# Kernel tuning notes

Hardware: AMD Instinct MI355X
Metric: run time of the kernel (lower is better)

Reference implementation:

```python
import jax, jax.numpy as jnp
import numpy as np
import math

B, T, C, H = 2, 2048, 1024, 16
D = C // H  # head dim = 64


def setup_inputs() -> dict:
    key = jax.random.key(0)
    ks = jax.random.split(key, 9)
    s = 1.0 / math.sqrt(C)
    inp = {
        "x": jax.random.normal(ks[0], (B, T, C), dtype=jnp.float32),
        "Wk": jax.random.normal(ks[1], (C, C), dtype=jnp.float32) * s,
        "bk": jax.random.normal(ks[2], (C,), dtype=jnp.float32) * s,
        "Wq": jax.random.normal(ks[3], (C, C), dtype=jnp.float32) * s,
        "bq": jax.random.normal(ks[4], (C,), dtype=jnp.float32) * s,
        "Wv": jax.random.normal(ks[5], (C, C), dtype=jnp.float32) * s,
        "bv": jax.random.normal(ks[6], (C,), dtype=jnp.float32) * s,
        "Wo": jax.random.normal(ks[7], (C, C), dtype=jnp.float32) * s,
        "bo": jax.random.normal(ks[8], (C,), dtype=jnp.float32) * s,
    }
    return inp


def reference(x, Wk, bk, Wq, bq, Wv, bv, Wo, bo):
    # QKV projections, split heads: [B,T,C] -> [B,H,T,D]
    def proj(W, b):
        return (x @ W.T + b).reshape(B, T, H, D).transpose(0, 2, 1, 3)

    k = proj(Wk, bk)
    q = proj(Wq, bq)
    v = proj(Wv, bv)

    # NOTE: original scales by 1/sqrt(embedding_dim), not head_dim
    scale = 1.0 / math.sqrt(C)
    scores = jnp.einsum("bhtd,bhsd->bhts", q, k) * scale  # [B,H,T,T]
    causal = jnp.tril(jnp.ones((T, T), dtype=bool))
    scores = jnp.where(causal[None, None], scores, -jnp.inf)
    attn = jax.nn.softmax(scores, axis=-1)
    y = jnp.einsum("bhts,bhsd->bhtd", attn, v)  # [B,H,T,D]
    y = y.transpose(0, 2, 1, 3).reshape(B, T, C)
    return y @ Wo.T + bo
```

## Files before the change

kernel.cpp:

```cpp
#include <hip/hip_runtime.h>
#include <hip/hip_bf16.h>
#include <stdint.h>
#include <stddef.h>

#define B_ 2
#define T_ 2048
#define C_ 1024
#define H_ 16
#define D_ 64
#define M_ (B_*T_)

typedef __attribute__((ext_vector_type(8))) short short8;
typedef __attribute__((ext_vector_type(4))) float f32x4;
typedef __attribute__((ext_vector_type(16))) float f32x16;
typedef __attribute__((ext_vector_type(4))) unsigned int u32x4;

__device__ __forceinline__ unsigned short f2bf(float f) {
    unsigned u = __float_as_uint(f);
    unsigned r = 0x7FFFu + ((u >> 16) & 1u);
    return (unsigned short)((u + r) >> 16);
}

__device__ __forceinline__ unsigned cvtpk_bf16(float lo, float hi) {
    unsigned r;
    asm("v_cvt_pk_bf16_f32 %0, %1, %2" : "=v"(r) : "v"(lo), "v"(hi));
    return r;
}

__device__ __forceinline__ float fexp2(float x) {
    float r;
    asm("v_exp_f32 %0, %1" : "=v"(r) : "v"(x));
    return r;
}

__device__ __forceinline__ void plswap(unsigned &a, unsigned &b) {
    asm("v_permlane32_swap_b32 %0, %1" : "+v"(a), "+v"(b));
}

__device__ __forceinline__ float xhalf_max(float v) {
    float a = v, b = v;
    asm("" : "+v"(b));
    asm("v_permlane32_swap_b32 %0, %1" : "+v"(a), "+v"(b));
    return fmaxf(a, b);
}
__device__ __forceinline__ float xhalf_sum(float v) {
    float a = v, b = v;
    asm("" : "+v"(b));
    asm("v_permlane32_swap_b32 %0, %1" : "+v"(a), "+v"(b));
    return a + b;
}

__device__ __forceinline__ void gload16(const void* g, void* l) {
    __builtin_amdgcn_global_load_lds(
        (__attribute__((address_space(1))) void*)g,
        (__attribute__((address_space(3))) void*)l,
        16, 0, 0);
}

__global__ void cvt_all(const float* __restrict__ x,  const float* __restrict__ wk,
                        const float* __restrict__ wq, const float* __restrict__ wv,
                        const float* __restrict__ wo,
                        unsigned short* __restrict__ xb,  unsigned short* __restrict__ wkb,
                        unsigned short* __restrict__ wqb, unsigned short* __restrict__ wvb,
                        unsigned short* __restrict__ wob) {
    int idx = (blockIdx.x * blockDim.x + threadIdx.x) * 4;
    const float* in; unsigned short* out; int off;
    if      (idx < (4<<20)) { in = x;  out = xb;  off = idx; }
    else if (idx < (5<<20)) { in = wk; out = wkb; off = idx - (4<<20); }
    else if (idx < (6<<20)) { in = wq; out = wqb; off = idx - (5<<20); }
    else if (idx < (7<<20)) { in = wv; out = wvb; off = idx - (6<<20); }
    else                    { in = wo; out = wob; off = idx - (7<<20); }
    float4 v = *reinterpret_cast<const float4*>(in + off);
    ushort4 o;
    o.x = f2bf(v.x); o.y = f2bf(v.y); o.z = f2bf(v.z); o.w = f2bf(v.w);
    *reinterpret_cast<ushort4*>(out + off) = o;
}

__global__ __launch_bounds__(256) void gemm_qkv(
    const unsigned short* __restrict__ A,
    const unsigned short* __restrict__ W0,
    const unsigned short* __restrict__ W1,
    const unsigned short* __restrict__ W2,
    const float* __restrict__ b0,
    const float* __restrict__ b1,
    const float* __restrict__ b2,
    unsigned short* __restrict__ o0,
    unsigned short* __restrict__ o1,
    unsigned short* __restrict__ o2)
{
    __shared__ unsigned short As[128*32];
    __shared__ unsigned short Bs[128*32];
    int which = blockIdx.x >> 8;
    int bx = blockIdx.x & 255;
    int bm = bx >> 3, bn = bx & 7;
    const unsigned short* W = (which==0) ? W0 : ((which==1) ? W1 : W2);
    const float* bias = (which==0) ? b0 : ((which==1) ? b1 : b2);

    int tid = threadIdx.x;
    int lane = tid & 63;
    int fr = lane & 15, fq = lane >> 4;
    int wid = tid >> 6;
    int wr = wid >> 1, wc = wid & 1;

    int srow = tid >> 2;
    int scol = (tid & 3) << 3;
    const unsigned short* Ab = A + (size_t)(bm*128 + srow) * C_ + scol;
    const unsigned short* Wb = W + (size_t)(bn*128 + srow) * C_ + scol;

    f32x4 acc[4][4] = {};

    for (int kt = 0; kt < C_/32; ++kt) {
        int ko = kt*32;
        gload16(Ab + ko,            &As[tid*8]);
        gload16(Ab + 64*C_ + ko,    &As[2048 + tid*8]);
        gload16(Wb + ko,            &Bs[tid*8]);
        gload16(Wb + 64*C_ + ko,    &Bs[2048 + tid*8]);
        __syncthreads();
        short8 af[4], bfr[4];
        #pragma unroll
        for (int i = 0; i < 4; ++i) {
            af[i]  = *reinterpret_cast<const short8*>(&As[(wr*64 + i*16 + fr)*32 + fq*8]);
            bfr[i] = *reinterpret_cast<const short8*>(&Bs[(wc*64 + i*16 + fr)*32 + fq*8]);
        }
        #pragma unroll
        for (int i = 0; i < 4; ++i)
            #pragma unroll
            for (int j = 0; j < 4; ++j)
                acc[i][j] = __builtin_amdgcn_mfma_f32_16x16x32_bf16(af[i], bfr[j], acc[i][j], 0, 0, 0);
        __syncthreads();
    }

    float sc = (which == 1) ? 0.045084220f : 1.0f;
    int mbase = bm*128 + wr*64;
    int nbase = bn*128 + wc*64;
    #pragma unroll
    for (int j = 0; j < 4; ++j) {
        int col = nbase + j*16 + fr;
        float bv = bias[col];
        int h = col >> 6, d = col & 63;
        #pragma unroll
        for (int i = 0; i < 4; ++i) {
            int r0 = mbase + i*16 + fq*4;
            #pragma unroll
            for (int r = 0; r < 4; ++r) {
                float v = (acc[i][j][r] + bv) * sc;
                int m = r0 + r;
                int b = m >> 11, t = m & (T_-1);
                unsigned short hv = f2bf(v);
                if (which == 2)
                    o2[((size_t)(b*H_ + h)*D_ + d)*T_ + t] = hv;
                else {
                    unsigned short* o = (which==0) ? o0 : o1;
                    o[((size_t)(b*H_ + h)*T_ + t)*D_ + d] = hv;
                }
            }
        }
    }
}

__global__ __launch_bounds__(256, 6) void gemm_out(
    const unsigned short* __restrict__ A,
    const unsigned short* __restrict__ W,
    const float* __restrict__ bias,
    float* __restrict__ out)
{
    __shared__ unsigned short As[64*32];
    __shared__ unsigned short Bs[128*32];
    int bx = blockIdx.x;
    int bm = bx >> 3, bn = bx & 7;

    int tid = threadIdx.x;
    int lane = tid & 63;
    int fr = lane & 15, fq = lane >> 4;
    int wid = tid >> 6;
    int wr = wid >> 1, wc = wid & 1;

    int arow = tid >> 2;
    int acol = (tid & 3) << 3;
    const unsigned short* Ab = A + (size_t)(bm*64 + arow) * C_ + acol;
    const unsigned short* Wb = W + (size_t)(bn*128 + arow) * C_ + acol;

    f32x4 acc[2][4] = {};

    for (int kt = 0; kt < C_/32; ++kt) {
        int ko = kt*32;
        gload16(Ab + ko,            &As[tid*8]);
        gload16(Wb + ko,            &Bs[tid*8]);
        gload16(Wb + 64*C_ + ko,    &Bs[2048 + tid*8]);
        __syncthreads();
        short8 af[2], bfr[4];
        #pragma unroll
        for (int i = 0; i < 2; ++i)
            af[i]  = *reinterpret_cast<const short8*>(&As[(wr*32 + i*16 + fr)*32 + fq*8]);
        #pragma unroll
        for (int j = 0; j < 4; ++j)
            bfr[j] = *reinterpret_cast<const short8*>(&Bs[(wc*64 + j*16 + fr)*32 + fq*8]);
        #pragma unroll
        for (int i = 0; i < 2; ++i)
            #pragma unroll
            for (int j = 0; j < 4; ++j)
                acc[i][j] = __builtin_amdgcn_mfma_f32_16x16x32_bf16(af[i], bfr[j], acc[i][j], 0, 0, 0);
        __syncthreads();
    }

    int mbase = bm*64 + wr*32;
    int nbase = bn*128 + wc*64;
    #pragma unroll
    for (int j = 0; j < 4; ++j) {
        int col = nbase + j*16 + fr;
        float bv = bias[col];
        #pragma unroll
        for (int i = 0; i < 2; ++i) {
            int r0 = mbase + i*16 + fq*4;
            #pragma unroll
            for (int r = 0; r < 4; ++r)
                out[(size_t)(r0 + r)*C_ + col] = acc[i][j][r] + bv;
        }
    }
}

__device__ __forceinline__ void attn_subtile(
    const short8 (&kf)[4], const short8 (&qf)[4],
    const short8 (&vlo)[2], const short8 (&vhi)[2],
    bool diag, int l31, int hi,
    f32x16& o0, f32x16& o1, float& m_, float& l_)
{
    f32x16 a0 = {};
    __builtin_amdgcn_s_setprio(1);
    a0 = __builtin_amdgcn_mfma_f32_32x32x16_bf16(kf[0], qf[0], a0, 0, 0, 0);
    a0 = __builtin_amdgcn_mfma_f32_32x32x16_bf16(kf[1], qf[1], a0, 0, 0, 0);
    a0 = __builtin_amdgcn_mfma_f32_32x32x16_bf16(kf[2], qf[2], a0, 0, 0, 0);
    a0 = __builtin_amdgcn_mfma_f32_32x32x16_bf16(kf[3], qf[3], a0, 0, 0, 0);
    __builtin_amdgcn_s_setprio(0);

    if (diag) {
        #pragma unroll
        for (int r = 0; r < 16; ++r) {
            int kvl = (r&3) + 8*(r>>2) + 4*hi;
            if (kvl > l31) a0[r] = -1e30f;
        }
    }

    float x0 = fmaxf(a0[0], a0[1]),   x1 = fmaxf(a0[2], a0[3]);
    float x2 = fmaxf(a0[4], a0[5]),   x3 = fmaxf(a0[6], a0[7]);
    float x4 = fmaxf(a0[8], a0[9]),   x5 = fmaxf(a0[10], a0[11]);
    float x6 = fmaxf(a0[12], a0[13]), x7 = fmaxf(a0[14], a0[15]);
    float y0 = fmaxf(x0, x1), y1 = fmaxf(x2, x3), y2 = fmaxf(x4, x5), y3 = fmaxf(x6, x7);
    float pm = fmaxf(fmaxf(y0, y1), fmaxf(y2, y3));
    pm = xhalf_max(pm);

    if (!__all(pm - m_ <= 8.0f)) {
        float mn = fmaxf(m_, pm);
        float alpha = fexp2(m_ - mn);
        l_ *= alpha;
        m_ = mn;
        #pragma unroll
        for (int r = 0; r < 16; ++r) {
            int row = (r&3) + 8*(r>>2) + 4*hi;
            float ar = __shfl(alpha, row);
            o0[r] *= ar;
            o1[r] *= ar;
        }
    }

    #pragma unroll
    for (int r = 0; r < 16; ++r)
        a0[r] = fexp2(a0[r] - m_);
    float s0 = a0[0]+a0[1],  s1 = a0[2]+a0[3],  s2 = a0[4]+a0[5],   s3 = a0[6]+a0[7];
    float s4 = a0[8]+a0[9],  s5 = a0[10]+a0[11], s6 = a0[12]+a0[13], s7 = a0[14]+a0[15];
    float u0 = s0+s1, u1 = s2+s3, u2 = s4+s5, u3 = s6+s7;
    float rs = (u0+u1) + (u2+u3);
    rs = xhalf_sum(rs);
    l_ += rs;

    unsigned pk_[8];
    #pragma unroll
    for (int jj = 0; jj < 8; ++jj)
        pk_[jj] = cvtpk_bf16(a0[2*jj], a0[2*jj+1]);

    #pragma unroll
    for (int kb = 0; kb < 2; ++kb) {
        unsigned fx = pk_[4*kb+0], fz = pk_[4*kb+2];
        unsigned fy = pk_[4*kb+1], fw = pk_[4*kb+3];
        plswap(fx, fz);
        plswap(fy, fw);
        u32x4 wv;
        wv.x = fx; wv.y = fy; wv.z = fz; wv.w = fw;
        short8 pfrag = __builtin_bit_cast(short8, wv);
        __builtin_amdgcn_s_setprio(1);
        o0 = __builtin_amdgcn_mfma_f32_32x32x16_bf16(pfrag, vlo[kb], o0, 0, 0, 0);
        o1 = __builtin_amdgcn_mfma_f32_32x32x16_bf16(pfrag, vhi[kb], o1, 0, 0, 0);
        __builtin_amdgcn_s_setprio(0);
    }
}

__global__ __launch_bounds__(256, 4) void flash_attn(
    const unsigned short* __restrict__ q,
    const unsigned short* __restrict__ k,
    const unsigned short* __restrict__ vt,
    unsigned short* __restrict__ y)
{
    __shared__ __align__(16) char LDSRAW[35840];
    unsigned short (*ST)[4][2048] = reinterpret_cast<unsigned short(*)[4][2048]>(LDSRAW);
    float* oP = reinterpret_cast<float*>(LDSRAW);
    float* mP = oP + 4*32*68;
    float* lP = mP + 128;

    int tid = threadIdx.x, lane = tid & 63, w = tid >> 6;
    int l31 = lane & 31, hi = lane >> 5, rsw = l31 & 7;
    int p = w & 1, s = w >> 1;
    int bid = blockIdx.x;

    int half = bid >> 9;
    int idx  = bid & 511;
    int bh   = (idx & 7)*4 + ((idx >> 3) & 3);
    int jidx = idx >> 5;
    int j    = half ? jidx : (31 - jidx);

    const unsigned short* kp = k  + (size_t)bh*T_*D_;
    const unsigned short* vp = vt + (size_t)bh*D_*T_;
    int b = bh >> 4, h = bh & 15;

    int rowbase = j*64 + p*32;
    const unsigned short* qp = q + ((size_t)bh*T_ + rowbase) * D_;

    short8 qf[4];
    #pragma unroll
    for (int dk = 0; dk < 4; ++dk)
        qf[dk] = *reinterpret_cast<const short8*>(qp + (size_t)l31*D_ + dk*16 + hi*8);

    f32x16 o0 = {}, o1 = {};
    float m_ = -1e30f, l_ = 0.f;

    int lim = 2*j + p;
    int niter = j + 1;
    int gbase = s ? (j + 1) : 0;

    #define STAGE(ii, bufi)                                                           \
    {                                                                                 \
        int c2 = tid;                                                                 \
        int krow = c2 >> 3;                                                           \
        int kslot = (c2 & 7) ^ (krow & 7);                                            \
        int vrow = c2 >> 2;                                                           \
        int vslot = (c2 & 3) ^ (vrow & 3);                                            \
        int tl_ = (ii), th_ = j + 1 + (ii);                                           \
        gload16(kp + ((size_t)(tl_*32 + krow))*D_ + kslot*8, &ST[bufi][0][c2*8]);     \
        gload16(kp + ((size_t)(th_*32 + krow))*D_ + kslot*8, &ST[bufi][1][c2*8]);     \
        gload16(vp + (size_t)vrow*T_ + tl_*32 + vslot*8,     &ST[bufi][2][c2*8]);     \
        gload16(vp + (size_t)vrow*T_ + th_*32 + vslot*8,     &ST[bufi][3][c2*8]);     \
    }

    STAGE(0, 0);
    __syncthreads();

    for (int i = 0; i < niter; ++i) {
        int bufi = i & 1;
        if (i + 1 < niter) STAGE(i + 1, bufi ^ 1);

        int g = gbase + i;
        if (g <= lim) {
            const unsigned short* Kl = &ST[bufi][s][0];
            const unsigned short* Vl = &ST[bufi][2 + s][0];
            short8 kf[4];
            #pragma unroll
            for (int dk = 0; dk < 4; ++dk)
                kf[dk] = *reinterpret_cast<const short8*>(
                    Kl + l31*64 + ((((dk<<1)|hi)) ^ rsw)*8);
            short8 vlo[2], vhi[2];
            #pragma unroll
            for (int kb = 0; kb < 2; ++kb) {
                int sl = ((((kb<<1)|hi)) ^ (l31 & 3)) * 8;
                vlo[kb] = *reinterpret_cast<const short8*>(Vl + l31*32 + sl);
                vhi[kb] = *reinterpret_cast<const short8*>(Vl + (32 + l31)*32 + sl);
            }
            attn_subtile(kf, qf, vlo, vhi, g == lim, l31, hi, o0, o1, m_, l_);
        }
        __syncthreads();
    }
    #undef STAGE

    {
        int set = (s << 1) | p;
        #pragma unroll
        for (int rr = 0; rr < 16; ++rr) {
            int crow = (rr&3) + 8*(rr>>2) + 4*hi;
            oP[(set*32 + crow)*68 + l31]      = o0[rr];
            oP[(set*32 + crow)*68 + 32 + l31] = o1[rr];
        }
        if (!hi) { mP[set*32 + l31] = m_; lP[set*32 + l31] = l_; }
    }
    __syncthreads();
    {
        int qr = tid >> 3;
        int dc = tid & 7;
        #pragma unroll
        for (int ch = 0; ch < 2; ++ch) {
            int sA = ch, sB = 2 + ch;
            float mA = mP[sA*32 + qr], mB = mP[sB*32 + qr];
            float lA = lP[sA*32 + qr], lB = lP[sB*32 + qr];
            float mN = fmaxf(mA, mB);
            float aA = fexp2(mA - mN);
            float aB = fexp2(mB - mN);
            float lN = lA*aA + lB*aB;
            float inv = 1.0f / lN;
            float cA = aA * inv, cB = aB * inv;

            unsigned short yv[8];
            #pragma unroll
            for (int e = 0; e < 8; ++e) {
                float acc = cA * oP[(sA*32 + qr)*68 + dc*8 + e]
                          + cB * oP[(sB*32 + qr)*68 + dc*8 + e];
                yv[e] = f2bf(acc);
            }
            int trow = j*64 + ch*32 + qr;
            size_t base = ((size_t)(b*T_ + trow))*C_ + h*64 + dc*8;
            *reinterpret_cast<short8*>(y + base) = *reinterpret_cast<short8*>(yv);
        }
    }
}

extern "C" void kernel_launch(void* const* d_in, const int* in_sizes, int n_in,
                              void* d_out, int out_size, void* d_ws, size_t ws_size,
                              hipStream_t stream) {
    const float* x  = (const float*)d_in[0];
    const float* Wk = (const float*)d_in[1];
    const float* bk = (const float*)d_in[2];
    const float* Wq = (const float*)d_in[3];
    const float* bq = (const float*)d_in[4];
    const float* Wv = (const float*)d_in[5];
    const float* bv = (const float*)d_in[6];
    const float* Wo = (const float*)d_in[7];
    const float* bo = (const float*)d_in[8];
    float* out = (float*)d_out;

    char* ws = (char*)d_ws;
    unsigned short* xb  = (unsigned short*)(ws);
    unsigned short* wkb = (unsigned short*)(ws + ((size_t)8  << 20));
    unsigned short* wqb = (unsigned short*)(ws + ((size_t)10 << 20));
    unsigned short* wvb = (unsigned short*)(ws + ((size_t)12 << 20));
    unsigned short* wob = (unsigned short*)(ws + ((size_t)14 << 20));
    unsigned short* qb  = (unsigned short*)(ws + ((size_t)16 << 20));
    unsigned short* kb  = (unsigned short*)(ws + ((size_t)24 << 20));
    unsigned short* vtb = (unsigned short*)(ws + ((size_t)32 << 20));
    unsigned short* yb  = (unsigned short*)(ws + ((size_t)40 << 20));

    cvt_all<<<dim3(8192), dim3(256), 0, stream>>>(
        x, Wk, Wq, Wv, Wo, xb, wkb, wqb, wvb, wob);

    gemm_qkv<<<dim3(768), dim3(256), 0, stream>>>(xb, wkb, wqb, wvb, bk, bq, bv, kb, qb, vtb);

    flash_attn<<<dim3(1024), dim3(256), 0, stream>>>(qb, kb, vtb, yb);

    gemm_out<<<dim3(512), dim3(256), 0, stream>>>(yb, wob, bo, out);
}
```

Baseline: 102.9 us.

## Double-buffer QKV GEMM shared tiles and remap block order

The QKV projection GEMM now uses two shared-memory buffers, so the global-to-LDS load for the next K tile is issued before the MFMAs on the current tile. This removes one barrier per iteration and lets memory latency overlap compute. Block indices are also permuted, presumably to spread related tiles across XCDs for cache locality. Shared memory doubles to 32KB per block, which may reduce occupancy, and with a single barrier per iteration the correctness of reusing a buffer depends on the async-load ordering semantics of gload16.

```diff
diff --git a/kernel.cpp b/kernel.cpp
--- a/kernel.cpp
+++ b/kernel.cpp
@@ -88,10 +88,13 @@
     unsigned short* __restrict__ o1,
     unsigned short* __restrict__ o2)
 {
-    __shared__ unsigned short As[128*32];
-    __shared__ unsigned short Bs[128*32];
-    int which = blockIdx.x >> 8;
-    int bx = blockIdx.x & 255;
+    __shared__ unsigned short As[2][128*32];
+    __shared__ unsigned short Bs[2][128*32];
+
+    int bid = blockIdx.x;
+    int nb = (bid & 7) * 96 + (bid >> 3);
+    int which = nb >> 8;
+    int bx = nb & 255;
     int bm = bx >> 3, bn = bx & 7;
     const unsigned short* W = (which==0) ? W0 : ((which==1) ? W1 : W2);
     const float* bias = (which==0) ? b0 : ((which==1) ? b1 : b2);
@@ -109,18 +112,27 @@
 
     f32x4 acc[4][4] = {};
 
+    #define QKV_STAGE(kt_, bf_)                                        \
+    {                                                                  \
+        int ko_ = (kt_)*32;                                            \
+        gload16(Ab + ko_,            &As[bf_][tid*8]);                 \
+        gload16(Ab + 64*C_ + ko_,    &As[bf_][2048 + tid*8]);          \
+        gload16(Wb + ko_,            &Bs[bf_][tid*8]);                 \
+        gload16(Wb + 64*C_ + ko_,    &Bs[bf_][2048 + tid*8]);         \
+    }
+
+    QKV_STAGE(0, 0);
+    __syncthreads();
+
     for (int kt = 0; kt < C_/32; ++kt) {
-        int ko = kt*32;
-        gload16(Ab + ko,            &As[tid*8]);
-        gload16(Ab + 64*C_ + ko,    &As[2048 + tid*8]);
-        gload16(Wb + ko,            &Bs[tid*8]);
-        gload16(Wb + 64*C_ + ko,    &Bs[2048 + tid*8]);
-        __syncthreads();
+        int buf = kt & 1;
+        if (kt + 1 < C_/32) QKV_STAGE(kt + 1, buf ^ 1);
+
         short8 af[4], bfr[4];
         #pragma unroll
         for (int i = 0; i < 4; ++i) {
-            af[i]  = *reinterpret_cast<const short8*>(&As[(wr*64 + i*16 + fr)*32 + fq*8]);
-            bfr[i] = *reinterpret_cast<const short8*>(&Bs[(wc*64 + i*16 + fr)*32 + fq*8]);
+            af[i]  = *reinterpret_cast<const short8*>(&As[buf][(wr*64 + i*16 + fr)*32 + fq*8]);
+            bfr[i] = *reinterpret_cast<const short8*>(&Bs[buf][(wc*64 + i*16 + fr)*32 + fq*8]);
         }
         #pragma unroll
         for (int i = 0; i < 4; ++i)
@@ -129,6 +141,7 @@
                 acc[i][j] = __builtin_amdgcn_mfma_f32_16x16x32_bf16(af[i], bfr[j], acc[i][j], 0, 0, 0);
         __syncthreads();
     }
+    #undef QKV_STAGE
 
     float sc = (which == 1) ? 0.045084220f : 1.0f;
     int mbase = bm*128 + wr*64;
```

Result: slower. 118.5 us (+15.2%).
